# Kernel optimization log

Hardware: AMD Instinct MI355X
Metric: run time of the kernel (lower is better)

## Reference

```python
import jax, jax.numpy as jnp
import numpy as np


def setup_inputs() -> dict:
    key = jax.random.key(0)
    k1, k2, k3, k4, k5 = jax.random.split(key, 5)
    B, C, T, N = 32, 1024, 1024, 3
    video = jax.random.normal(k1, (B, C, T, 1, 1), dtype=jnp.float32)
    length = jax.random.randint(k2, (B,), 1, T + 1).astype(jnp.int32)
    center = 0.5 * jax.random.normal(k3, (N,), dtype=jnp.float32)
    delta = 0.01 * jax.random.normal(k4, (N,), dtype=jnp.float32)
    gamma = 0.0001 * jax.random.normal(k5, (N,), dtype=jnp.float32)
    return {"video": video, "length": length, "center": center,
            "delta": delta, "gamma": gamma}


def reference(video, length, center, delta, gamma):
    B, C, T = video.shape[0], video.shape[1], video.shape[2]
    N = center.shape[0]
    v = video.reshape(B, C, T)
    c = jnp.tanh(center)                                  # (N,)
    g = jnp.tanh(gamma)                                   # (N,)
    lf = length.astype(jnp.float32)                       # (B,)
    # per-(batch, filter) Cauchy center; delta is multiplied by zeros in the
    # original code and therefore has no effect on the output.
    centers = (lf[:, None] - 1.0) * (c[None, :] + 1.0) / 2.0   # (B, N)
    gammas = jnp.exp(1.5 - 2.0 * jnp.abs(g))              # (N,)
    t = jnp.arange(T, dtype=jnp.float32)                  # (T,)
    diff = (t[None, None, :] - centers[:, :, None]) / gammas[None, :, None]
    f = 1.0 / (jnp.pi * gammas[None, :, None] * (1.0 + diff * diff))  # (B,N,T)
    f = f / (jnp.sum(f, axis=2, keepdims=True) + 1e-6)
    # pooled output: for each batch/channel, N weighted time-averages
    o = jnp.einsum('bnt,bct->bcn', f, v)                  # (B, C, N)
    return o.reshape(B, C * N)
```

## Files before the change

### kernel.cpp

```cpp
#include <hip/hip_runtime.h>
#include <math.h>

constexpr int B = 32;
constexpr int C = 1024;
constexpr int T = 1024;
constexpr int N = 3;

__global__ __launch_bounds__(256) void tsf_weights(
    const int* __restrict__ length,
    const float* __restrict__ center,
    const float* __restrict__ gamma_,
    float* __restrict__ f ) {
  const int bn = blockIdx.x;
  const int b = bn / N;
  const int n = bn % N;

  const float c = tanhf(center[n]);
  const float g = tanhf(gamma_[n]);
  const float lf = (float)length[b];
  const float ctr = (lf - 1.0f) * (c + 1.0f) * 0.5f;
  const float gam = expf(1.5f - 2.0f * fabsf(g));
  const float inv_gam = 1.0f / gam;
  const float pref = 1.0f / (3.14159265358979f * gam);

  float vals[4];
  float s = 0.0f;
#pragma unroll
  for (int i = 0; i < 4; ++i) {
    const float t = (float)(threadIdx.x + i * 256);
    const float d = (t - ctr) * inv_gam;
    vals[i] = pref / (1.0f + d * d);
    s += vals[i];
  }

#pragma unroll
  for (int off = 32; off > 0; off >>= 1) s += __shfl_down(s, off);

  __shared__ float wsum[4];
  const int lane = threadIdx.x & 63;
  const int wv = threadIdx.x >> 6;
  if (lane == 0) wsum[wv] = s;
  __syncthreads();
  const float tot = wsum[0] + wsum[1] + wsum[2] + wsum[3];
  const float inv = 1.0f / (tot + 1e-6f);

  float* frow = f + (size_t)bn * T;
#pragma unroll
  for (int i = 0; i < 4; ++i) frow[threadIdx.x + i * 256] = vals[i] * inv;
}

constexpr int CPB = 16;

__global__ __launch_bounds__(256) void tsf_pool(
    const float* __restrict__ v ,
    const float* __restrict__ f ,
    float* __restrict__ out ) {
  const int groups_per_b = C / CPB;
  const int b = blockIdx.x / groups_per_b;
  const int cg = blockIdx.x % groups_per_b;

  __shared__ float fs[N][T];

  {
    const float4* src = (const float4*)(f + (size_t)b * N * T);
    float4* dst = (float4*)(&fs[0][0]);
#pragma unroll
    for (int i = threadIdx.x; i < (N * T) / 4; i += 256) dst[i] = src[i];
  }
  __syncthreads();

  const int lane = threadIdx.x & 63;
  const int wv = threadIdx.x >> 6;

  const float4* w0 = (const float4*)(&fs[0][0]);
  const float4* w1 = (const float4*)(&fs[1][0]);
  const float4* w2 = (const float4*)(&fs[2][0]);

  for (int cc = wv; cc < CPB; cc += 4) {
    const int ch = cg * CPB + cc;
    const float4* row = (const float4*)(v + ((size_t)b * C + ch) * T);

    float a0 = 0.f, a1 = 0.f, a2 = 0.f;
#pragma unroll
    for (int i = lane; i < T / 4; i += 64) {
      const float4 x = row[i];
      const float4 q0 = w0[i];
      const float4 q1 = w1[i];
      const float4 q2 = w2[i];
      a0 += x.x * q0.x + x.y * q0.y + x.z * q0.z + x.w * q0.w;
      a1 += x.x * q1.x + x.y * q1.y + x.z * q1.z + x.w * q1.w;
      a2 += x.x * q2.x + x.y * q2.y + x.z * q2.z + x.w * q2.w;
    }

#pragma unroll
    for (int off = 32; off > 0; off >>= 1) {
      a0 += __shfl_down(a0, off);
      a1 += __shfl_down(a1, off);
      a2 += __shfl_down(a2, off);
    }

    if (lane == 0) {
      float* o = out + ((size_t)b * C + ch) * N;
      o[0] = a0;
      o[1] = a1;
      o[2] = a2;
    }
  }
}

extern "C" void kernel_launch(void* const* d_in, const int* in_sizes, int n_in,
                              void* d_out, int out_size, void* d_ws,
                              size_t ws_size, hipStream_t stream) {
  const float* video = (const float*)d_in[0];
  const int* length = (const int*)d_in[1];
  const float* center = (const float*)d_in[2];
  const float* gamma_ = (const float*)d_in[4];
  float* out = (float*)d_out;

  float* f = (float*)d_ws;

  tsf_weights<<<B * N, 256, 0, stream>>>(length, center, gamma_, f);
  tsf_pool<<<B * (C / CPB), 256, 0, stream>>>(video, f, out);
}
```

Before: 32.28 us.

## Fuse Cauchy weight computation into pooling kernel, recomputing per block

The separate weights kernel and its workspace round trip are removed. Each pooling block now computes the three normalized Cauchy filters for its batch directly into shared memory before doing the dot products. This drops one launch and the global write and read of the weights, but every block redundantly evaluates 3x1024 weights plus tanh and exp, and adds a second barrier.

```diff
diff --git a/kernel.cpp b/kernel.cpp
--- a/kernel.cpp
+++ b/kernel.cpp
@@ -5,72 +5,59 @@
 constexpr int C = 1024;
 constexpr int T = 1024;
 constexpr int N = 3;
+constexpr int CPB = 16;
 
-__global__ __launch_bounds__(256) void tsf_weights(
+__global__ __launch_bounds__(256) void tsf_fused(
+    const float* __restrict__ v ,
     const int* __restrict__ length,
     const float* __restrict__ center,
     const float* __restrict__ gamma_,
-    float* __restrict__ f ) {
-  const int bn = blockIdx.x;
-  const int b = bn / N;
-  const int n = bn % N;
-
-  const float c = tanhf(center[n]);
-  const float g = tanhf(gamma_[n]);
-  const float lf = (float)length[b];
-  const float ctr = (lf - 1.0f) * (c + 1.0f) * 0.5f;
-  const float gam = expf(1.5f - 2.0f * fabsf(g));
-  const float inv_gam = 1.0f / gam;
-  const float pref = 1.0f / (3.14159265358979f * gam);
-
-  float vals[4];
-  float s = 0.0f;
-#pragma unroll
-  for (int i = 0; i < 4; ++i) {
-    const float t = (float)(threadIdx.x + i * 256);
-    const float d = (t - ctr) * inv_gam;
-    vals[i] = pref / (1.0f + d * d);
-    s += vals[i];
-  }
-
-#pragma unroll
-  for (int off = 32; off > 0; off >>= 1) s += __shfl_down(s, off);
-
-  __shared__ float wsum[4];
-  const int lane = threadIdx.x & 63;
-  const int wv = threadIdx.x >> 6;
-  if (lane == 0) wsum[wv] = s;
-  __syncthreads();
-  const float tot = wsum[0] + wsum[1] + wsum[2] + wsum[3];
-  const float inv = 1.0f / (tot + 1e-6f);
-
-  float* frow = f + (size_t)bn * T;
-#pragma unroll
-  for (int i = 0; i < 4; ++i) frow[threadIdx.x + i * 256] = vals[i] * inv;
-}
-
-constexpr int CPB = 16;
-
-__global__ __launch_bounds__(256) void tsf_pool(
-    const float* __restrict__ v ,
-    const float* __restrict__ f ,
     float* __restrict__ out ) {
   const int groups_per_b = C / CPB;
   const int b = blockIdx.x / groups_per_b;
   const int cg = blockIdx.x % groups_per_b;
 
   __shared__ float fs[N][T];
+  __shared__ float wsum[N][4];
 
-  {
-    const float4* src = (const float4*)(f + (size_t)b * N * T);
-    float4* dst = (float4*)(&fs[0][0]);
+  const int lane = threadIdx.x & 63;
+  const int wv = threadIdx.x >> 6;
+
+  const float lf = (float)length[b];
+
+  float vals[N][4];
 #pragma unroll
-    for (int i = threadIdx.x; i < (N * T) / 4; i += 256) dst[i] = src[i];
+  for (int n = 0; n < N; ++n) {
+    const float c = tanhf(center[n]);
+    const float g = tanhf(gamma_[n]);
+    const float ctr = (lf - 1.0f) * (c + 1.0f) * 0.5f;
+    const float gam = expf(1.5f - 2.0f * fabsf(g));
+    const float inv_gam = 1.0f / gam;
+    const float pref = 1.0f / (3.14159265358979f * gam);
+
+    float s = 0.0f;
+#pragma unroll
+    for (int i = 0; i < 4; ++i) {
+      const float t = (float)(threadIdx.x + i * 256);
+      const float d = (t - ctr) * inv_gam;
+      vals[n][i] = pref / (1.0f + d * d);
+      s += vals[n][i];
+    }
+#pragma unroll
+    for (int off = 32; off > 0; off >>= 1) s += __shfl_down(s, off);
+    if (lane == 0) wsum[n][wv] = s;
   }
   __syncthreads();
 
-  const int lane = threadIdx.x & 63;
-  const int wv = threadIdx.x >> 6;
+#pragma unroll
+  for (int n = 0; n < N; ++n) {
+    const float inv =
+        1.0f / (wsum[n][0] + wsum[n][1] + wsum[n][2] + wsum[n][3] + 1e-6f);
+#pragma unroll
+    for (int i = 0; i < 4; ++i)
+      fs[n][threadIdx.x + i * 256] = vals[n][i] * inv;
+  }
+  __syncthreads();
 
   const float4* w0 = (const float4*)(&fs[0][0]);
   const float4* w1 = (const float4*)(&fs[1][0]);
@@ -117,8 +104,6 @@
   const float* gamma_ = (const float*)d_in[4];
   float* out = (float*)d_out;
 
-  float* f = (float*)d_ws;
-
-  tsf_weights<<<B * N, 256, 0, stream>>>(length, center, gamma_, f);
-  tsf_pool<<<B * (C / CPB), 256, 0, stream>>>(video, f, out);
+  tsf_fused<<<B * (C / CPB), 256, 0, stream>>>(video, length, center, gamma_,
+                                               out);
 }
```

Result: faster. 30.00 us (-7.1%).
